# Kernel optimization log

Hardware: AMD Instinct MI355X
Metric: run time of the kernel (lower is better)

The kernel has to match this reference:

```python
import jax, jax.numpy as jnp
import numpy as np

N = 50000        # total nodes
E = 600000       # total edges (before self loops)
NID = 16         # node_input_dim
D = 128          # hidden_dim
H = 4            # heads
C = D // H       # out_channels per head = 32
L = 4            # num_layers
EPS = 1e-5
NEG_SLOPE = 0.2


def setup_inputs() -> dict:
    key = jax.random.key(0)
    ks = jax.random.split(key, 16)
    s = 0.05
    return {
        "node_types": jax.random.randint(ks[0], (N,), 0, 3),
        "edge_index": jax.random.randint(ks[1], (2, E), 0, N),
        # embedding + input projection (Linear -> LayerNorm -> ReLU)
        "emb_table": jax.random.normal(ks[2], (3, NID), jnp.float32) * s,
        "proj_W": jax.random.normal(ks[3], (NID, D), jnp.float32) * s,
        "proj_b": jnp.zeros((D,), jnp.float32),
        "proj_g": jnp.ones((D,), jnp.float32),
        "proj_beta": jnp.zeros((D,), jnp.float32),
        # per-layer GATv2 params (stacked over L layers)
        "Wl": jax.random.normal(ks[4], (L, D, D), jnp.float32) * s,   # lin_l weight
        "bl": jnp.zeros((L, D), jnp.float32),                          # lin_l bias
        "Wr": jax.random.normal(ks[5], (L, D, D), jnp.float32) * s,   # lin_r weight
        "br": jnp.zeros((L, D), jnp.float32),                          # lin_r bias
        "att": jax.random.normal(ks[6], (L, H, C), jnp.float32) * s,  # attention vector
        "gat_bias": jnp.zeros((L, D), jnp.float32),                   # output bias (concat)
        # per-layer LayerNorm
        "ln_g": jnp.ones((L, D), jnp.float32),
        "ln_b": jnp.zeros((L, D), jnp.float32),
    }


def layer_norm(x, g, b):
    mu = jnp.mean(x, axis=-1, keepdims=True)
    var = jnp.mean(jnp.square(x - mu), axis=-1, keepdims=True)
    return (x - mu) * jax.lax.rsqrt(var + EPS) * g + b


def gatv2_layer(x, src, dst, Wl, bl, Wr, br, att, bias):
    # x: [N, D]; src/dst: [E+N] (self loops included)
    n = x.shape[0]
    xl = (x @ Wl + bl).reshape(n, H, C)   # source transform
    xr = (x @ Wr + br).reshape(n, H, C)   # destination transform
    e = jax.nn.leaky_relu(xl[src] + xr[dst], NEG_SLOPE)          # [E', H, C]
    logits = jnp.einsum('ehc,hc->eh', e, att)                    # [E', H]
    m = jax.ops.segment_max(logits, dst, num_segments=n)         # segment softmax (stable)
    alpha = jnp.exp(logits - m[dst])
    denom = jax.ops.segment_sum(alpha, dst, num_segments=n)
    alpha = alpha / denom[dst]                                   # [E', H]
    msg = xl[src] * alpha[:, :, None]                            # [E', H, C]
    out = jax.ops.segment_sum(msg, dst, num_segments=n)          # [N, H, C]
    return out.reshape(n, H * C) + bias


def reference(node_types, edge_index, emb_table, proj_W, proj_b, proj_g, proj_beta,
              Wl, bl, Wr, br, att, gat_bias, ln_g, ln_b):
    n = node_types.shape[0]
    loop = jnp.arange(n, dtype=edge_index.dtype)
    src = jnp.concatenate([edge_index[0], loop])   # add self loops
    dst = jnp.concatenate([edge_index[1], loop])

    x = emb_table[node_types]                      # [N, NID]
    x = jax.nn.relu(layer_norm(x @ proj_W + proj_b, proj_g, proj_beta))  # input_proj (dropout=id at eval)

    for i in range(L):
        x_res = x
        x = gatv2_layer(x, src, dst, Wl[i], bl[i], Wr[i], br[i], att[i], gat_bias[i])
        x = layer_norm(x + x_res, ln_g[i], ln_b[i])
        x = jax.nn.relu(x)
    return x
```

## Files before the change

kernel.cpp:

```cpp
#include <hip/hip_runtime.h>
#include <hip/hip_bf16.h>
#include <math.h>

#define D      128
#define NID    16
#define H      4
#define CH     32
#define NLAYER 4
#define EPS    1e-5f
#define NEG    0.2f
#define LOG2E  1.442695040888963f
#define SRCMASK 0x0FFFFFFF

typedef __attribute__((ext_vector_type(8))) short short8;
typedef __attribute__((ext_vector_type(4))) float floatx4;
typedef _Float16 h2 __attribute__((ext_vector_type(2)));
typedef float fx2 __attribute__((ext_vector_type(2)));

__device__ __forceinline__ float2 bf2_to_f2(unsigned int u) {
    float2 r;
    unsigned int lo = u << 16;
    unsigned int hi = u & 0xffff0000u;
    r.x = __uint_as_float(lo);
    r.y = __uint_as_float(hi);
    return r;
}

__device__ __forceinline__ unsigned short f2bf(float f) {
    __hip_bfloat16 h = __float2bfloat16(f);
    return *reinterpret_cast<unsigned short*>(&h);
}

__device__ __forceinline__ unsigned short f2h(float f) {
    _Float16 h = (_Float16)f;
    unsigned short u;
    __builtin_memcpy(&u, &h, 2);
    return u;
}

__device__ __forceinline__ h2 u2h2(unsigned int u) {
    h2 v;
    __builtin_memcpy(&v, &u, 4);
    return v;
}

__device__ __forceinline__ h2 pkrtz(float a, float b) {
    auto r = __builtin_amdgcn_cvt_pkrtz(a, b);
    h2 out;
    __builtin_memcpy(&out, &r, 4);
    return out;
}

__device__ __forceinline__ unsigned char f2fp8(float v) {
    int pk = __builtin_amdgcn_cvt_pk_fp8_f32(v, v, 0, false);
    return (unsigned char)(pk & 0xff);
}

__device__ __forceinline__ void fp8x4_to_h2x2(unsigned int w, h2* out) {
    fx2 f0 = __builtin_amdgcn_cvt_pk_f32_fp8((int)w, false);
    fx2 f1 = __builtin_amdgcn_cvt_pk_f32_fp8((int)w, true);
    out[0] = pkrtz(f0[0], f0[1]);
    out[1] = pkrtz(f1[0], f1[1]);
}


__global__ __launch_bounds__(256) void scan_blocks_kernel(const int* __restrict__ deg, int* __restrict__ offs,
                                                          int* __restrict__ bsum, int n) {
    __shared__ int sw[8];
    int t = threadIdx.x;
    int i = blockIdx.x * 256 + t;
    int v = (i < n) ? deg[i] + 1 : 0;
    int lane = t & 63, w = t >> 6;
    int x = v;
    #pragma unroll
    for (int off = 1; off < 64; off <<= 1) {
        int y = __shfl_up(x, off, 64);
        if (lane >= off) x += y;
    }
    if (lane == 63) sw[w] = x;
    __syncthreads();
    if (t == 0) {
        int s = 0;
        for (int k = 0; k < 4; ++k) { int tv = sw[k]; sw[k] = s; s += tv; }
        sw[4] = s;
    }
    __syncthreads();
    int excl = x - v + sw[w];
    if (i < n) offs[i] = excl;
    if (t == 255) bsum[blockIdx.x] = sw[4];
}

__global__ __launch_bounds__(256) void scan_add_kernel(int* __restrict__ offs, const int* __restrict__ bsum,
                                                       int* __restrict__ cursor, int n, int nb, int total) {
    __shared__ int sw[8];
    __shared__ int sS;
    int t = threadIdx.x;
    int bid = blockIdx.x;
    int v = (t < bid && t < nb) ? bsum[t] : 0;
    int lane = t & 63, w = t >> 6;
    #pragma unroll
    for (int off = 32; off > 0; off >>= 1) v += __shfl_xor(v, off, 64);
    if (lane == 0) sw[w] = v;
    __syncthreads();
    if (t == 0) sS = sw[0] + sw[1] + sw[2] + sw[3];
    __syncthreads();
    int S = sS;
    int i = bid * 256 + t;
    if (i < n) {
        int o = offs[i] + S;
        offs[i] = o;
        cursor[i] = o;
    }
    if (i == 0) offs[n] = total;
}

__global__ __launch_bounds__(256) void scatter_kernel(
    const int* __restrict__ srcs, const int* __restrict__ dsts,
    const int* __restrict__ types,
    int e, int n, int* cursor, int* __restrict__ csr_src) {
    int i = blockIdx.x * blockDim.x + threadIdx.x;
    if (i < e) {
        int s = srcs[i];
        int ty = types[s];
        int pos = atomicAdd(&cursor[dsts[i]], 1);
        csr_src[pos] = s | (ty << 28);
    } else if (i < e + n) {
        int node = i - e;
        int ty = types[node];
        int pos = atomicAdd(&cursor[node], 1);
        csr_src[pos] = node | (ty << 28);
    }
}

__global__ __launch_bounds__(256) void setup_kernel(
    const float* __restrict__ emb,
    const float* __restrict__ W, const float* __restrict__ pb,
    const float* __restrict__ pg, const float* __restrict__ pbeta,
    const float* __restrict__ Wl, const float* __restrict__ Wr,
    const float* __restrict__ bl, const float* __restrict__ br,
    unsigned short* __restrict__ wt,
    const int* __restrict__ dsts, int* __restrict__ deg, int e,
    unsigned short* __restrict__ x3bf, unsigned char* __restrict__ xl3,
    unsigned short* __restrict__ xr3,
    int nbE) {
    __shared__ float sbuf[NID * D];
    __shared__ float semb[3 * NID];
    int blk = blockIdx.x;
    int t = threadIdx.x;
    if (blk < 512) {
        int idx = blk * 256 + t;
        int k    = idx & (D - 1);
        int nrow = (idx >> 7) & (D - 1);
        int s    = (idx >> 14) & 1;
        int l    = idx >> 15;
        const float* Wm = s ? Wr : Wl;
        wt[idx] = f2bf(Wm[(size_t)l * D * D + (size_t)k * D + nrow]);
    } else if (blk < 512 + nbE) {
        int i = (blk - 512) * 256 + t;
        if (i < e) atomicAdd(&deg[dsts[i]], 1);
    } else {
        float* p3  = sbuf;
        float* x3s = sbuf + 384;
        float* red = sbuf + 768;
        for (int i = t; i < 3 * NID; i += 256) semb[i] = emb[i];
        __syncthreads();
        int c = t;
        if (c < D) {
            float wcol[NID];
            #pragma unroll
            for (int k = 0; k < NID; ++k) wcol[k] = W[k * D + c];
            float bc = pb[c];
            #pragma unroll
            for (int ty = 0; ty < 3; ++ty) {
                float a = bc;
                #pragma unroll
                for (int k = 0; k < NID; ++k) a = fmaf(semb[ty * NID + k], wcol[k], a);
                p3[ty * D + c] = a;
            }
        }
        __syncthreads();
        #pragma unroll 1
        for (int ty = 0; ty < 3; ++ty) {
            float v = (c < D) ? p3[ty * D + c] : 0.0f;
            float s = v, sq = v * v;
            #pragma unroll
            for (int off = 1; off < 64; off <<= 1) {
                s  += __shfl_xor(s, off, 64);
                sq += __shfl_xor(sq, off, 64);
            }
            if ((t & 63) == 0 && t < 128) { red[(t >> 6) * 2] = s; red[(t >> 6) * 2 + 1] = sq; }
            __syncthreads();
            float S = red[0] + red[2], SQ = red[1] + red[3];
            float mu = S * (1.0f / D), var = SQ * (1.0f / D) - mu * mu;
            float r = rsqrtf(var + EPS);
            if (c < D) {
                float o = fmaxf((p3[ty * D + c] - mu) * r * pg[c] + pbeta[c], 0.0f);
                unsigned short bfv = f2bf(o);
                x3s[ty * D + c] = __uint_as_float((unsigned int)bfv << 16);
                x3bf[ty * D + c] = bfv;
            }
            __syncthreads();
        }
        if (c < D) {
            #pragma unroll 1
            for (int ty = 0; ty < 3; ++ty) {
                float al = bl[c], ar = br[c];
                for (int k = 0; k < D; ++k) {
                    float xv = x3s[ty * D + k];
                    al = fmaf(xv, Wl[(size_t)k * D + c], al);
                    ar = fmaf(xv, Wr[(size_t)k * D + c], ar);
                }
                xl3[ty * D + c] = f2fp8(al);
                xr3[ty * D + c] = f2h(ar);
            }
        }
    }
}

__global__ __launch_bounds__(256) void dual_gemm_mfma_kernel(
    const unsigned short* __restrict__ x, const unsigned short* __restrict__ wt,
    const float* __restrict__ bl, const float* __restrict__ br,
    unsigned char* __restrict__ xl, unsigned short* __restrict__ xr, int n) {
    __shared__ __align__(16) unsigned short sa[64 * 136];
    int t = threadIdx.x;
    int nbase = blockIdx.x * 64;
    int rows = n - nbase; if (rows > 64) rows = 64;
    int lane = t & 63, w = t >> 6;
    int L = lane & 15, q = lane >> 4;
    int s  = w >> 1;
    int n0 = (w & 1) * 64;
    const unsigned short* wb = wt + ((size_t)s * D + n0) * D;
    short8 b[4][4];
    #pragma unroll
    for (int kk = 0; kk < 4; ++kk)
        #pragma unroll
        for (int ni = 0; ni < 4; ++ni)
            b[kk][ni] = *(const short8*)(wb + (size_t)(ni * 16 + L) * D + kk * 32 + q * 8);
    {
        int r   = t >> 2;
        int seg = t & 3;
        uint4* drow = (uint4*)(sa + r * 136 + seg * 32);
        if (r < rows) {
            const uint4* srow = (const uint4*)(x + (size_t)(nbase + r) * D + seg * 32);
            drow[0] = srow[0]; drow[1] = srow[1]; drow[2] = srow[2]; drow[3] = srow[3];
        } else {
            uint4 z = make_uint4(0, 0, 0, 0);
            drow[0] = z; drow[1] = z; drow[2] = z; drow[3] = z;
        }
    }
    __syncthreads();
    floatx4 acc[4][4];
    #pragma unroll
    for (int mi = 0; mi < 4; ++mi)
        #pragma unroll
        for (int ni = 0; ni < 4; ++ni)
            acc[mi][ni] = (floatx4){0.0f, 0.0f, 0.0f, 0.0f};
    #pragma unroll
    for (int kk = 0; kk < 4; ++kk) {
        int ko = kk * 32 + q * 8;
        short8 a[4];
        #pragma unroll
        for (int mi = 0; mi < 4; ++mi)
            a[mi] = *(const short8*)(sa + (mi * 16 + L) * 136 + ko);
        #pragma unroll
        for (int mi = 0; mi < 4; ++mi)
            #pragma unroll
            for (int ni = 0; ni < 4; ++ni)
                acc[mi][ni] = __builtin_amdgcn_mfma_f32_16x16x32_bf16(a[mi], b[kk][ni], acc[mi][ni], 0, 0, 0);
    }
    const float* bias = s ? br : bl;
    __syncthreads();
    if (s == 0) {
        unsigned char* sb = (unsigned char*)sa;
        #pragma unroll
        for (int ni = 0; ni < 4; ++ni) {
            int col = n0 + ni * 16 + L;
            float bv = bias[col];
            #pragma unroll
            for (int mi = 0; mi < 4; ++mi) {
                #pragma unroll
                for (int r = 0; r < 4; ++r) {
                    int row = mi * 16 + q * 4 + r;
                    sb[row * 272 + col] = f2fp8(acc[mi][ni][r] + bv);
                }
            }
        }
    }
    __syncthreads();
    {
        unsigned char* sb = (unsigned char*)sa;
        #pragma unroll
        for (int c = 0; c < 2; ++c) {
            int chunk = c * 256 + t;
            int row   = chunk >> 3;
            int off   = (chunk & 7) * 16;
            if (row < rows) {
                uint4 v = *(const uint4*)(sb + row * 272 + off);
                *(uint4*)(xl + (size_t)(nbase + row) * D + off) = v;
            }
        }
    }
    __syncthreads();
    if (s == 1) {
        #pragma unroll
        for (int ni = 0; ni < 4; ++ni) {
            int col = n0 + ni * 16 + L;
            float bv = bias[col];
            #pragma unroll
            for (int mi = 0; mi < 4; ++mi) {
                #pragma unroll
                for (int r = 0; r < 4; ++r) {
                    int row = mi * 16 + q * 4 + r;
                    sa[row * 136 + col] = f2h(acc[mi][ni][r] + bv);
                }
            }
        }
    }
    __syncthreads();
    #pragma unroll
    for (int c = 0; c < 4; ++c) {
        int chunk = c * 256 + t;
        int row   = chunk >> 4;
        int off   = (chunk & 15) * 8;
        if (row < rows) {
            short8 v = *(const short8*)(sa + row * 136 + off);
            *(short8*)(xr + (size_t)(nbase + row) * D + off) = v;
        }
    }
}

template<bool L0>
__global__ __launch_bounds__(256) void gat_agg_kernel(
    const unsigned char* __restrict__ xl, const unsigned short* __restrict__ xr,
    const unsigned short* __restrict__ xin,
    const unsigned char* __restrict__ xl3, const unsigned short* __restrict__ xr3,
    const unsigned short* __restrict__ x3bf, const int* __restrict__ types,
    const int* __restrict__ offs, const int* __restrict__ csr_src,
    const float* __restrict__ att,
    const float* __restrict__ gbias,
    const float* __restrict__ lng, const float* __restrict__ lnb,
    unsigned short* __restrict__ xout_bf, float* __restrict__ xout_f32, int n) {
    int t = threadIdx.x;
    int lane = t & 63, w = t >> 6;
    int node = blockIdx.x * 4 + w;
    if (node >= n) return;
    int g  = lane >> 4;
    int l  = lane & 15;
    int cb = l * 8;
    int tyn = L0 ? types[node] : 0;
    const unsigned short* xrrow = L0 ? (xr3 + (size_t)tyn * D) : (xr + (size_t)node * D);
    h2 xr2[4], at2[4];
    {
        uint4 u = *(const uint4*)(xrrow + cb);
        xr2[0] = u2h2(u.x); xr2[1] = u2h2(u.y); xr2[2] = u2h2(u.z); xr2[3] = u2h2(u.w);
        float4 t0 = *(const float4*)(att + cb);
        float4 t1 = *(const float4*)(att + cb + 4);
        at2[0] = (h2){(_Float16)(t0.x * LOG2E), (_Float16)(t0.y * LOG2E)};
        at2[1] = (h2){(_Float16)(t0.z * LOG2E), (_Float16)(t0.w * LOG2E)};
        at2[2] = (h2){(_Float16)(t1.x * LOG2E), (_Float16)(t1.y * LOG2E)};
        at2[3] = (h2){(_Float16)(t1.z * LOG2E), (_Float16)(t1.w * LOG2E)};
    }
    auto rowp = [&](int v) -> const unsigned char* {
        if (L0) return xl3 + (size_t)((v >> 28) & 3) * D;
        return xl + (size_t)(v & SRCMASK) * D;
    };
    h2 acch[4];
    #pragma unroll
    for (int i = 0; i < 4; ++i) acch[i] = (h2){(_Float16)0.0f, (_Float16)0.0f};
    float lsum = 0.0f;
    int s0 = offs[node], s1 = offs[node + 1];
    int j0 = s0 + g;
    bool val_c = j0 < s1;
    int src_c = csr_src[val_c ? j0 : s0];
    uint2 u_c = *(const uint2*)(rowp(src_c) + cb);
    int j1 = j0 + 4;
    bool val_n = j1 < s1;
    int src_n = csr_src[val_n ? j1 : s0];
    uint2 u_n = *(const uint2*)(rowp(src_n) + cb);
    int j2 = j0 + 8;
    bool val_2 = j2 < s1;
    int src_2 = csr_src[val_2 ? j2 : s0];
    for (int j = s0; j < s1; j += 4) {
        uint2 u_2 = *(const uint2*)(rowp(src_2) + cb);
        int j3 = j + 12 + g;
        bool val_3 = j3 < s1;
        int src_3 = csr_src[val_3 ? j3 : s0];
        h2 xv2[4];
        fp8x4_to_h2x2(u_c.x, xv2);
        fp8x4_to_h2x2(u_c.y, xv2 + 2);
        float p = 0.0f;
        #pragma unroll
        for (int i = 0; i < 4; ++i) {
            h2 e  = xv2[i] + xr2[i];
            h2 el = __builtin_elementwise_max(e, e * (_Float16)NEG);
            p = __builtin_amdgcn_fdot2(el, at2[i], p, false);
        }
        p += __shfl_xor(p, 1, 64);
        p += __shfl_xor(p, 2, 64);
        float wgt = val_c ? exp2f(p) : 0.0f;
        lsum += wgt;
        _Float16 wh = (_Float16)wgt;
        h2 w2 = {wh, wh};
        #pragma unroll
        for (int i = 0; i < 4; ++i) acch[i] += w2 * xv2[i];
        u_c = u_n; u_n = u_2;
        val_c = val_n; val_n = val_2;
        val_2 = val_3; src_2 = src_3;
    }
    float acc[8];
    #pragma unroll
    for (int i = 0; i < 4; ++i) {
        acc[2 * i]     = (float)acch[i][0];
        acc[2 * i + 1] = (float)acch[i][1];
    }
    #pragma unroll
    for (int i = 0; i < 8; ++i) {
        acc[i] += __shfl_xor(acc[i], 16, 64);
        acc[i] += __shfl_xor(acc[i], 32, 64);
    }
    lsum += __shfl_xor(lsum, 16, 64);
    lsum += __shfl_xor(lsum, 32, 64);
    float inv = 1.0f / lsum;
    const unsigned short* xinrow = L0 ? (x3bf + (size_t)tyn * D) : (xin + (size_t)node * D);
    float xi[8];
    {
        uint4 u = *(const uint4*)(xinrow + cb);
        float2 a = bf2_to_f2(u.x), b = bf2_to_f2(u.y), c = bf2_to_f2(u.z), d = bf2_to_f2(u.w);
        xi[0]=a.x; xi[1]=a.y; xi[2]=b.x; xi[3]=b.y; xi[4]=c.x; xi[5]=c.y; xi[6]=d.x; xi[7]=d.y;
    }
    float4 gb0 = *(const float4*)(gbias + cb);
    float4 gb1 = *(const float4*)(gbias + cb + 4);
    float gb[8] = {gb0.x, gb0.y, gb0.z, gb0.w, gb1.x, gb1.y, gb1.z, gb1.w};
    float v[8];
    #pragma unroll
    for (int i = 0; i < 8; ++i) v[i] = fmaf(acc[i], inv, gb[i] + xi[i]);
    float s = 0.0f, sq = 0.0f;
    #pragma unroll
    for (int i = 0; i < 8; ++i) { s += v[i]; sq = fmaf(v[i], v[i], sq); }
    #pragma unroll
    for (int off = 1; off < 16; off <<= 1) {
        s  += __shfl_xor(s, off, 64);
        sq += __shfl_xor(sq, off, 64);
    }
    float mu  = s * (1.0f / D);
    float var = sq * (1.0f / D) - mu * mu;
    float r   = rsqrtf(var + EPS);
    float4 lg0 = *(const float4*)(lng + cb);
    float4 lg1 = *(const float4*)(lng + cb + 4);
    float4 lb0 = *(const float4*)(lnb + cb);
    float4 lb1 = *(const float4*)(lnb + cb + 4);
    float lg[8] = {lg0.x, lg0.y, lg0.z, lg0.w, lg1.x, lg1.y, lg1.z, lg1.w};
    float lb[8] = {lb0.x, lb0.y, lb0.z, lb0.w, lb1.x, lb1.y, lb1.z, lb1.w};
    float o[8];
    #pragma unroll
    for (int i = 0; i < 8; ++i) o[i] = fmaxf((v[i] - mu) * r * lg[i] + lb[i], 0.0f);
    if (g == 0) {
        if (xout_f32) {
            *(float4*)(xout_f32 + (size_t)node * D + cb)     = make_float4(o[0], o[1], o[2], o[3]);
            *(float4*)(xout_f32 + (size_t)node * D + cb + 4) = make_float4(o[4], o[5], o[6], o[7]);
        } else {
            unsigned int p0 = (unsigned int)f2bf(o[0]) | ((unsigned int)f2bf(o[1]) << 16);
            unsigned int p1 = (unsigned int)f2bf(o[2]) | ((unsigned int)f2bf(o[3]) << 16);
            unsigned int p2 = (unsigned int)f2bf(o[4]) | ((unsigned int)f2bf(o[5]) << 16);
            unsigned int p3 = (unsigned int)f2bf(o[6]) | ((unsigned int)f2bf(o[7]) << 16);
            *(uint4*)(xout_bf + (size_t)node * D + cb) = make_uint4(p0, p1, p2, p3);
        }
    }
}

extern "C" void kernel_launch(void* const* d_in, const int* in_sizes, int n_in,
                              void* d_out, int out_size, void* d_ws, size_t ws_size,
                              hipStream_t stream) {
    const int*   node_types = (const int*)d_in[0];
    const int*   edge_index = (const int*)d_in[1];
    const float* emb        = (const float*)d_in[2];
    const float* projW      = (const float*)d_in[3];
    const float* projb      = (const float*)d_in[4];
    const float* projg      = (const float*)d_in[5];
    const float* projbeta   = (const float*)d_in[6];
    const float* Wl         = (const float*)d_in[7];
    const float* bl         = (const float*)d_in[8];
    const float* Wr         = (const float*)d_in[9];
    const float* br         = (const float*)d_in[10];
    const float* att        = (const float*)d_in[11];
    const float* gbias      = (const float*)d_in[12];
    const float* lng        = (const float*)d_in[13];
    const float* lnb        = (const float*)d_in[14];
    float* out = (float*)d_out;

    int n = in_sizes[0];
    int e = in_sizes[1] / 2;
    const int* srcs = edge_index;
    const int* dsts = edge_index + e;

    char* p = (char*)d_ws;
    auto carve = [&](size_t bytes) {
        char* q = p;
        p += (bytes + 255) & ~(size_t)255;
        return q;
    };
    int*   deg     = (int*)carve((size_t)n * 4);
    int*   offs    = (int*)carve((size_t)(n + 1) * 4);
    int*   cursor  = (int*)carve((size_t)n * 4);
    int*   bsum    = (int*)carve(256 * 4);
    int*   csr_src = (int*)carve((size_t)(e + n) * 4);
    unsigned short* xbuf = (unsigned short*)carve((size_t)n * D * 2);
    unsigned char*  xlb  = (unsigned char*)carve((size_t)n * D);
    unsigned short* xrb  = (unsigned short*)carve((size_t)n * D * 2);
    unsigned short* wt   = (unsigned short*)carve((size_t)NLAYER * 2 * D * D * 2);
    unsigned short* x3bf = (unsigned short*)carve(3 * D * 2);
    unsigned char*  xl3  = (unsigned char*)carve(3 * D);
    unsigned short* xr3  = (unsigned short*)carve(3 * D * 2);

    int nb = (n + 255) / 256;
    int nbE = (e + 255) / 256;
    int ntiles = (n + 63) / 64;
    int nscat  = (e + n + 255) / 256;

    hipMemsetAsync(deg, 0, (size_t)n * 4, stream);

    setup_kernel<<<512 + nbE + 1, 256, 0, stream>>>(
        emb, projW, projb, projg, projbeta,
        Wl, Wr, bl, br, wt, dsts, deg, e,
        x3bf, xl3, xr3, nbE);

    scan_blocks_kernel<<<nb, 256, 0, stream>>>(deg, offs, bsum, n);
    scan_add_kernel<<<nb, 256, 0, stream>>>(offs, bsum, cursor, n, nb, e + n);
    scatter_kernel<<<nscat, 256, 0, stream>>>(srcs, dsts, node_types, e, n, cursor, csr_src);

    gat_agg_kernel<true><<<(n + 3) / 4, 256, 0, stream>>>(
        xlb, xrb, xbuf, xl3, xr3, x3bf, node_types, offs, csr_src,
        att, gbias, lng, lnb, xbuf, nullptr, n);

    for (int layer = 1; layer < NLAYER; ++layer) {
        dual_gemm_mfma_kernel<<<ntiles, 256, 0, stream>>>(
            xbuf, wt + (size_t)layer * 2 * D * D,
            bl + (size_t)layer * D, br + (size_t)layer * D, xlb, xrb, n);
        bool last = (layer == NLAYER - 1);
        gat_agg_kernel<false><<<(n + 3) / 4, 256, 0, stream>>>(
            xlb, xrb, xbuf, xl3, xr3, x3bf, node_types, offs, csr_src,
            att + (size_t)layer * H * CH, gbias + (size_t)layer * D,
            lng + (size_t)layer * D, lnb + (size_t)layer * D,
            last ? (unsigned short*)nullptr : xbuf, last ? out : (float*)nullptr, n);
    }
}
```

Before: 353.2 us.

## Compute layer-0 attention densely from per-type neighbor counts and fuse CSR scatter

In layer 0 every node's features depend only on its type, so attention weights depend only on the (destination type, source type) pair. Setup now precomputes the nine per-head exp weights and counts each node's incoming edges per source type, packed as three 10-bit fields in the degree word. A per-node dense kernel then computes the layer-0 output without walking any edges. The CSR scatter is moved into the layer-1 GEMM launch as extra blocks, and the source-type tag is dropped from the CSR entries. The trade-off is that per-type in-degree must stay below 1024 or the packed counts overflow.

New measurement: 328.1 us. 7.1% less time.

```diff
diff --git a/kernel.cpp b/kernel.cpp
--- a/kernel.cpp
+++ b/kernel.cpp
@@ -10,7 +10,7 @@
 #define EPS    1e-5f
 #define NEG    0.2f
 #define LOG2E  1.442695040888963f
-#define SRCMASK 0x0FFFFFFF
+#define CNTMASK 1023
 
 typedef __attribute__((ext_vector_type(8))) short short8;
 typedef __attribute__((ext_vector_type(4))) float floatx4;
@@ -69,7 +69,11 @@
     __shared__ int sw[8];
     int t = threadIdx.x;
     int i = blockIdx.x * 256 + t;
-    int v = (i < n) ? deg[i] + 1 : 0;
+    int v = 0;
+    if (i < n) {
+        int d = deg[i];
+        v = (d & CNTMASK) + ((d >> 10) & CNTMASK) + ((d >> 20) & CNTMASK) + 1;
+    }
     int lane = t & 63, w = t >> 6;
     int x = v;
     #pragma unroll
@@ -114,36 +118,20 @@
     if (i == 0) offs[n] = total;
 }
 
-__global__ __launch_bounds__(256) void scatter_kernel(
-    const int* __restrict__ srcs, const int* __restrict__ dsts,
-    const int* __restrict__ types,
-    int e, int n, int* cursor, int* __restrict__ csr_src) {
-    int i = blockIdx.x * blockDim.x + threadIdx.x;
-    if (i < e) {
-        int s = srcs[i];
-        int ty = types[s];
-        int pos = atomicAdd(&cursor[dsts[i]], 1);
-        csr_src[pos] = s | (ty << 28);
-    } else if (i < e + n) {
-        int node = i - e;
-        int ty = types[node];
-        int pos = atomicAdd(&cursor[node], 1);
-        csr_src[pos] = node | (ty << 28);
-    }
-}
-
 __global__ __launch_bounds__(256) void setup_kernel(
     const float* __restrict__ emb,
     const float* __restrict__ W, const float* __restrict__ pb,
     const float* __restrict__ pg, const float* __restrict__ pbeta,
     const float* __restrict__ Wl, const float* __restrict__ Wr,
     const float* __restrict__ bl, const float* __restrict__ br,
+    const float* __restrict__ att,
     unsigned short* __restrict__ wt,
-    const int* __restrict__ dsts, int* __restrict__ deg, int e,
-    unsigned short* __restrict__ x3bf, unsigned char* __restrict__ xl3,
-    unsigned short* __restrict__ xr3,
+    const int* __restrict__ srcs, const int* __restrict__ dsts,
+    const int* __restrict__ types, int* __restrict__ deg, int e,
+    unsigned short* __restrict__ x3bf, float* __restrict__ xl3f,
+    float* __restrict__ w9,
     int nbE) {
-    __shared__ float sbuf[NID * D];
+    __shared__ float sbuf[2048];
     __shared__ float semb[3 * NID];
     int blk = blockIdx.x;
     int t = threadIdx.x;
@@ -157,11 +145,16 @@
         wt[idx] = f2bf(Wm[(size_t)l * D * D + (size_t)k * D + nrow]);
     } else if (blk < 512 + nbE) {
         int i = (blk - 512) * 256 + t;
-        if (i < e) atomicAdd(&deg[dsts[i]], 1);
+        if (i < e) {
+            int ty = types[srcs[i]];
+            atomicAdd(&deg[dsts[i]], 1 << (10 * ty));
+        }
     } else {
         float* p3  = sbuf;
         float* x3s = sbuf + 384;
         float* red = sbuf + 768;
+        float* xlf = sbuf + 772;
+        float* xrf = sbuf + 1156;
         for (int i = t; i < 3 * NID; i += 256) semb[i] = emb[i];
         __syncthreads();
         int c = t;
@@ -210,19 +203,98 @@
                     al = fmaf(xv, Wl[(size_t)k * D + c], al);
                     ar = fmaf(xv, Wr[(size_t)k * D + c], ar);
                 }
-                xl3[ty * D + c] = f2fp8(al);
-                xr3[ty * D + c] = f2h(ar);
-            }
-        }
+                xlf[ty * D + c] = al;
+                xrf[ty * D + c] = ar;
+                xl3f[ty * D + c] = al;
+            }
+        }
+        __syncthreads();
+        if (c < D) {
+            float av = att[c];
+            int h = c >> 5;
+            #pragma unroll 1
+            for (int tyd = 0; tyd < 3; ++tyd) {
+                #pragma unroll 1
+                for (int tys = 0; tys < 3; ++tys) {
+                    float ev = xlf[tys * D + c] + xrf[tyd * D + c];
+                    ev = fmaxf(ev, NEG * ev);
+                    float p = av * ev;
+                    #pragma unroll
+                    for (int off = 1; off < 32; off <<= 1) p += __shfl_xor(p, off, 32);
+                    if ((c & 31) == 0) w9[(tyd * 3 + tys) * H + h] = exp2f(p * LOG2E);
+                }
+            }
+        }
+    }
+}
+
+__global__ __launch_bounds__(256) void gat_l0_dense_kernel(
+    const int* __restrict__ deg, const int* __restrict__ types,
+    const float* __restrict__ w9, const float* __restrict__ xl3f,
+    const unsigned short* __restrict__ x3bf,
+    const float* __restrict__ gbias,
+    const float* __restrict__ lng, const float* __restrict__ lnb,
+    unsigned short* __restrict__ xout, int n, int ngrp) {
+    int t = threadIdx.x;
+    int lane = t & 63, w = t >> 6;
+    int c0 = 2 * lane;
+    int h = c0 >> 5;
+    for (int grp = blockIdx.x; grp < ngrp; grp += gridDim.x) {
+        int node = grp * 4 + w;
+        if (node >= n) continue;
+        int tyn = types[node];
+        int d = deg[node];
+        float cnt[3];
+        cnt[0] = (float)(d & CNTMASK);
+        cnt[1] = (float)((d >> 10) & CNTMASK);
+        cnt[2] = (float)((d >> 20) & CNTMASK);
+        cnt[tyn] += 1.0f;
+        float cw0 = cnt[0] * w9[(tyn * 3 + 0) * H + h];
+        float cw1 = cnt[1] * w9[(tyn * 3 + 1) * H + h];
+        float cw2 = cnt[2] * w9[(tyn * 3 + 2) * H + h];
+        float inv = 1.0f / (cw0 + cw1 + cw2);
+        float n0 = cw0 * xl3f[0 * D + c0] + cw1 * xl3f[1 * D + c0] + cw2 * xl3f[2 * D + c0];
+        float n1 = cw0 * xl3f[0 * D + c0 + 1] + cw1 * xl3f[1 * D + c0 + 1] + cw2 * xl3f[2 * D + c0 + 1];
+        float2 xi = bf2_to_f2(*(const unsigned int*)(x3bf + (size_t)tyn * D + c0));
+        float v0 = fmaf(n0, inv, gbias[c0]     + xi.x);
+        float v1 = fmaf(n1, inv, gbias[c0 + 1] + xi.y);
+        float s = v0 + v1, sq = v0 * v0 + v1 * v1;
+        #pragma unroll
+        for (int off = 1; off < 64; off <<= 1) {
+            s  += __shfl_xor(s, off, 64);
+            sq += __shfl_xor(sq, off, 64);
+        }
+        float mu  = s * (1.0f / D);
+        float var = sq * (1.0f / D) - mu * mu;
+        float r   = rsqrtf(var + EPS);
+        v0 = fmaxf((v0 - mu) * r * lng[c0]     + lnb[c0],     0.0f);
+        v1 = fmaxf((v1 - mu) * r * lng[c0 + 1] + lnb[c0 + 1], 0.0f);
+        unsigned int packed = (unsigned int)f2bf(v0) | ((unsigned int)f2bf(v1) << 16);
+        *(unsigned int*)(xout + (size_t)node * D + c0) = packed;
     }
 }
 
 __global__ __launch_bounds__(256) void dual_gemm_mfma_kernel(
     const unsigned short* __restrict__ x, const unsigned short* __restrict__ wt,
     const float* __restrict__ bl, const float* __restrict__ br,
-    unsigned char* __restrict__ xl, unsigned short* __restrict__ xr, int n) {
+    unsigned char* __restrict__ xl, unsigned short* __restrict__ xr, int n,
+    int ntiles,
+    const int* __restrict__ srcs, const int* __restrict__ dsts, int e,
+    int* __restrict__ cursor, int* __restrict__ csr_src) {
     __shared__ __align__(16) unsigned short sa[64 * 136];
     int t = threadIdx.x;
+    if (blockIdx.x >= ntiles) {
+        int i = (blockIdx.x - ntiles) * 256 + t;
+        if (i < e) {
+            int pos = atomicAdd(&cursor[dsts[i]], 1);
+            csr_src[pos] = srcs[i];
+        } else if (i < e + n) {
+            int node = i - e;
+            int pos = atomicAdd(&cursor[node], 1);
+            csr_src[pos] = node;
+        }
+        return;
+    }
     int nbase = blockIdx.x * 64;
     int rows = n - nbase; if (rows > 64) rows = 64;
     int lane = t & 63, w = t >> 6;
@@ -329,12 +401,9 @@
     }
 }
 
-template<bool L0>
 __global__ __launch_bounds__(256) void gat_agg_kernel(
     const unsigned char* __restrict__ xl, const unsigned short* __restrict__ xr,
     const unsigned short* __restrict__ xin,
-    const unsigned char* __restrict__ xl3, const unsigned short* __restrict__ xr3,
-    const unsigned short* __restrict__ x3bf, const int* __restrict__ types,
     const int* __restrict__ offs, const int* __restrict__ csr_src,
     const float* __restrict__ att,
     const float* __restrict__ gbias,
@@ -347,11 +416,9 @@
     int g  = lane >> 4;
     int l  = lane & 15;
     int cb = l * 8;
-    int tyn = L0 ? types[node] : 0;
-    const unsigned short* xrrow = L0 ? (xr3 + (size_t)tyn * D) : (xr + (size_t)node * D);
     h2 xr2[4], at2[4];
     {
-        uint4 u = *(const uint4*)(xrrow + cb);
+        uint4 u = *(const uint4*)(xr + (size_t)node * D + cb);
         xr2[0] = u2h2(u.x); xr2[1] = u2h2(u.y); xr2[2] = u2h2(u.z); xr2[3] = u2h2(u.w);
         float4 t0 = *(const float4*)(att + cb);
         float4 t1 = *(const float4*)(att + cb + 4);
@@ -360,10 +427,6 @@
         at2[2] = (h2){(_Float16)(t1.x * LOG2E), (_Float16)(t1.y * LOG2E)};
         at2[3] = (h2){(_Float16)(t1.z * LOG2E), (_Float16)(t1.w * LOG2E)};
     }
-    auto rowp = [&](int v) -> const unsigned char* {
-        if (L0) return xl3 + (size_t)((v >> 28) & 3) * D;
-        return xl + (size_t)(v & SRCMASK) * D;
-    };
     h2 acch[4];
     #pragma unroll
     for (int i = 0; i < 4; ++i) acch[i] = (h2){(_Float16)0.0f, (_Float16)0.0f};
@@ -372,16 +435,16 @@
     int j0 = s0 + g;
     bool val_c = j0 < s1;
     int src_c = csr_src[val_c ? j0 : s0];
-    uint2 u_c = *(const uint2*)(rowp(src_c) + cb);
+    uint2 u_c = *(const uint2*)(xl + (size_t)src_c * D + cb);
     int j1 = j0 + 4;
     bool val_n = j1 < s1;
     int src_n = csr_src[val_n ? j1 : s0];
-    uint2 u_n = *(const uint2*)(rowp(src_n) + cb);
+    uint2 u_n = *(const uint2*)(xl + (size_t)src_n * D + cb);
     int j2 = j0 + 8;
     bool val_2 = j2 < s1;
     int src_2 = csr_src[val_2 ? j2 : s0];
     for (int j = s0; j < s1; j += 4) {
-        uint2 u_2 = *(const uint2*)(rowp(src_2) + cb);
+        uint2 u_2 = *(const uint2*)(xl + (size_t)src_2 * D + cb);
         int j3 = j + 12 + g;
         bool val_3 = j3 < s1;
         int src_3 = csr_src[val_3 ? j3 : s0];
@@ -421,10 +484,9 @@
     lsum += __shfl_xor(lsum, 16, 64);
     lsum += __shfl_xor(lsum, 32, 64);
     float inv = 1.0f / lsum;
-    const unsigned short* xinrow = L0 ? (x3bf + (size_t)tyn * D) : (xin + (size_t)node * D);
     float xi[8];
     {
-        uint4 u = *(const uint4*)(xinrow + cb);
+        uint4 u = *(const uint4*)(xin + (size_t)node * D + cb);
         float2 a = bf2_to_f2(u.x), b = bf2_to_f2(u.y), c = bf2_to_f2(u.z), d = bf2_to_f2(u.w);
         xi[0]=a.x; xi[1]=a.y; xi[2]=b.x; xi[3]=b.y; xi[4]=c.x; xi[5]=c.y; xi[6]=d.x; xi[7]=d.y;
     }
@@ -509,36 +571,38 @@
     unsigned short* xrb  = (unsigned short*)carve((size_t)n * D * 2);
     unsigned short* wt   = (unsigned short*)carve((size_t)NLAYER * 2 * D * D * 2);
     unsigned short* x3bf = (unsigned short*)carve(3 * D * 2);
-    unsigned char*  xl3  = (unsigned char*)carve(3 * D);
-    unsigned short* xr3  = (unsigned short*)carve(3 * D * 2);
+    float*          xl3f = (float*)carve(3 * D * 4);
+    float*          w9   = (float*)carve(9 * H * 4);
 
     int nb = (n + 255) / 256;
     int nbE = (e + 255) / 256;
     int ntiles = (n + 63) / 64;
     int nscat  = (e + n + 255) / 256;
+    int ngrp   = (n + 3) / 4;
 
     hipMemsetAsync(deg, 0, (size_t)n * 4, stream);
 
     setup_kernel<<<512 + nbE + 1, 256, 0, stream>>>(
         emb, projW, projb, projg, projbeta,
-        Wl, Wr, bl, br, wt, dsts, deg, e,
-        x3bf, xl3, xr3, nbE);
+        Wl, Wr, bl, br, att, wt, srcs, dsts, node_types, deg, e,
+        x3bf, xl3f, w9, nbE);
 
     scan_blocks_kernel<<<nb, 256, 0, stream>>>(deg, offs, bsum, n);
     scan_add_kernel<<<nb, 256, 0, stream>>>(offs, bsum, cursor, n, nb, e + n);
-    scatter_kernel<<<nscat, 256, 0, stream>>>(srcs, dsts, node_types, e, n, cursor, csr_src);
-
-    gat_agg_kernel<true><<<(n + 3) / 4, 256, 0, stream>>>(
-        xlb, xrb, xbuf, xl3, xr3, x3bf, node_types, offs, csr_src,
-        att, gbias, lng, lnb, xbuf, nullptr, n);
+
+    gat_l0_dense_kernel<<<2048, 256, 0, stream>>>(
+        deg, node_types, w9, xl3f, x3bf,
+        gbias, lng, lnb, xbuf, n, ngrp);
 
     for (int layer = 1; layer < NLAYER; ++layer) {
-        dual_gemm_mfma_kernel<<<ntiles, 256, 0, stream>>>(
+        int extra = (layer == 1) ? nscat : 0;
+        dual_gemm_mfma_kernel<<<ntiles + extra, 256, 0, stream>>>(
             xbuf, wt + (size_t)layer * 2 * D * D,
-            bl + (size_t)layer * D, br + (size_t)layer * D, xlb, xrb, n);
+            bl + (size_t)layer * D, br + (size_t)layer * D, xlb, xrb, n,
+            ntiles, srcs, dsts, e, cursor, csr_src);
         bool last = (layer == NLAYER - 1);
-        gat_agg_kernel<false><<<(n + 3) / 4, 256, 0, stream>>>(
-            xlb, xrb, xbuf, xl3, xr3, x3bf, node_types, offs, csr_src,
+        gat_agg_kernel<<<ngrp, 256, 0, stream>>>(
+            xlb, xrb, xbuf, offs, csr_src,
             att + (size_t)layer * H * CH, gbias + (size_t)layer * D,
             lng + (size_t)layer * D, lnb + (size_t)layer * D,
             last ? (unsigned short*)nullptr : xbuf, last ? out : (float*)nullptr, n);
```
